# Performance work log

Measured on AMD Instinct MI355X. Metric: run time of the kernel, lower is better.

## Reference

```python
import jax, jax.numpy as jnp
import numpy as np

D_MODEL = 256   # per-head dim in this module
N_HEAD = 8
B, S = 4, 2048
NEG_INF = -1e9  # large negative in place of -inf for numerical safety


def setup_inputs() -> dict:
    key = jax.random.key(0)
    ks = jax.random.split(key, 8)
    d, h = D_MODEL, N_HEAD
    sc = 1.0 / np.sqrt(d)
    return {
        "Q": jax.random.normal(ks[0], (B, S, d), jnp.float32),
        "mask": jax.random.randint(ks[1], (B, S), 0, 2, jnp.int32),
        "WQ_w": jax.random.normal(ks[2], (h * d, d), jnp.float32) * sc,
        "WQ_b": jnp.zeros((h * d,), jnp.float32),
        "WK_w": jax.random.normal(ks[3], (h * d, d), jnp.float32) * sc,
        "WK_b": jnp.zeros((h * d,), jnp.float32),
        "WV_w": jax.random.normal(ks[4], (h * d, d), jnp.float32) * sc,
        "WV_b": jnp.zeros((h * d,), jnp.float32),
        "WO_w": jax.random.normal(ks[5], (d, h * d), jnp.float32) * sc,
        "WO_b": jnp.zeros((d,), jnp.float32),
        "ln_g": jnp.ones((d,), jnp.float32),
        "ln_b": jnp.zeros((d,), jnp.float32),
    }


def reference(Q, mask, WQ_w, WQ_b, WK_w, WK_b, WV_w, WV_b, WO_w, WO_b, ln_g, ln_b):
    b, s, d = Q.shape
    h = N_HEAD
    # projections (torch Linear: x @ W.T + b), split into heads: [b, h, s, d]
    q = (Q @ WQ_w.T + WQ_b).reshape(b, s, h, d).transpose(0, 2, 1, 3)
    k = (Q @ WK_w.T + WK_b).reshape(b, s, h, d).transpose(0, 2, 1, 3)
    v = (Q @ WV_w.T + WV_b).reshape(b, s, h, d).transpose(0, 2, 1, 3)
    # scaled dot-product scores [b, h, q, k]
    scores = jnp.einsum('bhqd,bhkd->bhqk', q, k) / jnp.sqrt(jnp.asarray(d, Q.dtype))
    key_mask = (mask != 0)[:, None, None, :]  # [b,1,1,k]
    scores = jnp.where(key_mask, scores, NEG_INF)
    alpha = jax.nn.softmax(scores, axis=-1)
    out = jnp.einsum('bhqk,bhkd->bhqd', alpha, v)
    out = out.transpose(0, 2, 1, 3).reshape(b, s, h * d)
    out = out @ WO_w.T + WO_b + Q  # dropout is identity in eval
    # LayerNorm over last dim
    mu = out.mean(-1, keepdims=True)
    var = out.var(-1, keepdims=True)
    return (out - mu) / jnp.sqrt(var + 1e-5) * ln_g + ln_b
```

## Files before the change

kernel.cpp:

```cpp
#include <hip/hip_runtime.h>
#include <cstddef>
#include <cstdint>

#define SQ 2048
#define DH 256
#define NH 8
#define BATCH 4
#define MROWS (BATCH*SQ)
#define HID (NH*DH)

typedef __attribute__((ext_vector_type(8)))  short bf16x8;
typedef __attribute__((ext_vector_type(16))) float f32x16;

typedef __attribute__((address_space(1))) const unsigned char gbuf_t;
typedef __attribute__((address_space(3))) unsigned char lbuf_t;

__device__ __forceinline__ void gl_lds16(const void* g, void* l) {
  __builtin_amdgcn_global_load_lds((gbuf_t*)g, (lbuf_t*)l, 16, 0, 0);
}

__device__ __forceinline__ unsigned short f2bf(float f) {
  unsigned u = __float_as_uint(f);
  unsigned r = (u + 0x7FFFu + ((u >> 16) & 1u)) >> 16;
  return (unsigned short)r;
}
__device__ __forceinline__ unsigned pk2(float a, float b) {
  return (unsigned)f2bf(a) | ((unsigned)f2bf(b) << 16);
}
__device__ __forceinline__ float fexp2(float x) {
  float r;
  asm("v_exp_f32 %0, %1" : "=v"(r) : "v"(x));
  return r;
}
__device__ __forceinline__ f32x16 zero16() {
  f32x16 v;
#pragma unroll
  for (int i = 0; i < 16; ++i) v[i] = 0.0f;
  return v;
}

__global__ void __launch_bounds__(256) cvt_kernel(
    const float* __restrict__ X,  const float* __restrict__ Wq,
    const float* __restrict__ Wk, const float* __restrict__ Wv,
    const float* __restrict__ Wo,
    unsigned short* __restrict__ Xb,  unsigned short* __restrict__ Wqb,
    unsigned short* __restrict__ Wkb, unsigned short* __restrict__ Wvb,
    unsigned short* __restrict__ Wob)
{
  int bid = blockIdx.x;
  const float* src; unsigned short* dst; size_t off;
  if      (bid < 512) { src = X;  dst = Xb;  off = (size_t)bid * 4096; }
  else if (bid < 640) { src = Wq; dst = Wqb; off = (size_t)(bid - 512) * 4096; }
  else if (bid < 768) { src = Wk; dst = Wkb; off = (size_t)(bid - 640) * 4096; }
  else if (bid < 896) { src = Wv; dst = Wvb; off = (size_t)(bid - 768) * 4096; }
  else                { src = Wo; dst = Wob; off = (size_t)(bid - 896) * 4096; }
  int tid = threadIdx.x;
#pragma unroll
  for (int k = 0; k < 4; ++k) {
    size_t idx = off + ((size_t)k * 256 + tid) * 4;
    float4 v = *(const float4*)(src + idx);
    uint2 o; o.x = pk2(v.x, v.y); o.y = pk2(v.z, v.w);
    *(uint2*)(dst + idx) = o;
  }
}

__global__ void __launch_bounds__(256, 2) qkv_kernel(
    const unsigned short* __restrict__ Xbf,
    const unsigned short* __restrict__ Wqb,
    const unsigned short* __restrict__ Wkb,
    const unsigned short* __restrict__ Wvb,
    const float* __restrict__ bq, const float* __restrict__ bk, const float* __restrict__ bv,
    unsigned short* __restrict__ q_ws, unsigned short* __restrict__ k_ws,
    unsigned short* __restrict__ vt_ws)
{
  __shared__ unsigned char TA[32768];
  __shared__ unsigned char TB[32768];
  const int tid = threadIdx.x, w = tid >> 6, l = tid & 63;
  const int h = l >> 5, t = l & 31;
  const int wm = w >> 1, wn = w & 1;
  const int z = blockIdx.z;
  const int m0 = (z == 2) ? blockIdx.y * 128 : blockIdx.x * 128;
  const int n0 = (z == 2) ? blockIdx.x * 128 : blockIdx.y * 128;
  const unsigned short* Asrc = (z == 2) ? Wvb : Xbf;
  const unsigned short* Bsrc = (z == 0) ? Wqb : (z == 1) ? Wkb : Xbf;

  const int rowo = l >> 4;
  const int bin  = (l & 15) * 16;
  const int swz  = (t & 15) << 4;

  f32x16 acc00 = zero16(), acc01 = zero16(), acc10 = zero16(), acc11 = zero16();

  for (int chunk = 0; chunk < 2; ++chunk) {
    __syncthreads();
#pragma unroll
    for (int i2 = 0; i2 < 8; ++i2) {
      int j = 8 * w + i2;
      int row = 4 * j + rowo;
      gl_lds16((const unsigned char*)(Asrc + (size_t)(m0 + row) * 256 + chunk * 128)
                 + (bin ^ ((row & 15) << 4)),
               &TA[j * 1024]);
    }
#pragma unroll
    for (int i2 = 0; i2 < 8; ++i2) {
      int j = 8 * w + i2;
      int row = 4 * j + rowo;
      gl_lds16((const unsigned char*)(Bsrc + (size_t)(n0 + row) * 256 + chunk * 128)
                 + (bin ^ ((row & 15) << 4)),
               &TB[j * 1024]);
    }
    __syncthreads();
#pragma unroll
    for (int kc = 0; kc < 8; ++kc) {
      int kb = (32 * kc + 16 * h) ^ swz;
      bf16x8 a0 = *(const bf16x8*)&TA[(size_t)(64 * wm + t) * 256 + kb];
      bf16x8 a1 = *(const bf16x8*)&TA[(size_t)(64 * wm + 32 + t) * 256 + kb];
      bf16x8 b0 = *(const bf16x8*)&TB[(size_t)(64 * wn + t) * 256 + kb];
      bf16x8 b1 = *(const bf16x8*)&TB[(size_t)(64 * wn + 32 + t) * 256 + kb];
      acc00 = __builtin_amdgcn_mfma_f32_32x32x16_bf16(a0, b0, acc00, 0, 0, 0);
      acc01 = __builtin_amdgcn_mfma_f32_32x32x16_bf16(a0, b1, acc01, 0, 0, 0);
      acc10 = __builtin_amdgcn_mfma_f32_32x32x16_bf16(a1, b0, acc10, 0, 0, 0);
      acc11 = __builtin_amdgcn_mfma_f32_32x32x16_bf16(a1, b1, acc11, 0, 0, 0);
    }
  }

  if (z < 2) {
    unsigned short* outp = z ? k_ws : q_ws;
    const float* bias = z ? bk : bq;
    float bn0 = bias[n0 + 64 * wn + t];
    float bn1 = bias[n0 + 64 * wn + 32 + t];
#pragma unroll
    for (int mt = 0; mt < 2; ++mt) {
#pragma unroll
      for (int nt = 0; nt < 2; ++nt) {
        int n = n0 + 64 * wn + 32 * nt + t;
        int headn = n >> 8, d = n & 255;
        float bb = nt ? bn1 : bn0;
        const f32x16& A = (mt == 0) ? (nt == 0 ? acc00 : acc01) : (nt == 0 ? acc10 : acc11);
#pragma unroll
        for (int r = 0; r < 16; ++r) {
          int m = m0 + 64 * wm + 32 * mt + (r & 3) + 8 * (r >> 2) + 4 * h;
          int batch = m >> 11, s = m & 2047;
          outp[(((size_t)batch * NH + headn) * SQ + s) * DH + d] = f2bf(A[r] + bb);
        }
      }
    }
  } else {
#pragma unroll
    for (int mt = 0; mt < 2; ++mt) {
#pragma unroll
      for (int r = 0; r < 16; ++r) {
        int j = m0 + 64 * wm + 32 * mt + (r & 3) + 8 * (r >> 2) + 4 * h;
        float bj = bv[j];
        int headj = j >> 8, jl = j & 255;
#pragma unroll
        for (int nt = 0; nt < 2; ++nt) {
          int sall = n0 + 64 * wn + 32 * nt + t;
          int batch = sall >> 11, ss = sall & 2047;
          const f32x16& A = (mt == 0) ? (nt == 0 ? acc00 : acc01) : (nt == 0 ? acc10 : acc11);
          vt_ws[((size_t)batch * NH + headj) * DH * SQ + (size_t)jl * SQ + ss] = f2bf(A[r] + bj);
        }
      }
    }
  }
}

__global__ void __launch_bounds__(512, 2) attn_kernel(
    const unsigned short* __restrict__ q_ws,
    const unsigned short* __restrict__ k_ws,
    const unsigned short* __restrict__ vt_ws,
    const int* __restrict__ mask,
    unsigned short* __restrict__ o_ws)
{
  __shared__ unsigned char KT[2][32768];
  __shared__ unsigned char VT[2][32768];
  __shared__ float MB[2048];

  const int tid = threadIdx.x, w = tid >> 6, l = tid & 63;
  const int h = l >> 5, t = l & 31;
  const int bid = blockIdx.x;
  const int xcd = bid & 7, slot = bid >> 3;
  const int bh = xcd * 4 + (slot >> 3);
  const int qt = slot & 7;
  const int b = bh >> 3, head = bh & 7;
  const int q0 = qt * 256;

  const float SC2 = 0.0625f * 1.44269504f;
  const float THR = 11.54f;

  {
    const int* mrow = mask + b * SQ;
    for (int i = tid; i < SQ; i += 512) MB[i] = mrow[i] ? 0.0f : -1.0e9f;
  }

  const unsigned short* kplane = k_ws + (size_t)bh * SQ * DH;
  const unsigned short* vplane = vt_ws + (size_t)bh * DH * SQ;

  bf16x8 qf[16];
  {
    const unsigned short* qb = q_ws + ((size_t)bh * SQ + (q0 + 32 * w + t)) * DH + 8 * h;
#pragma unroll
    for (int kc = 0; kc < 16; ++kc) qf[kc] = *(const bf16x8*)(qb + 16 * kc);
  }

  const int krow_o = l >> 5, kcol = (l & 31) * 16;
  const int vrow_o = l >> 3, vcol = (l & 7) * 16;

  {
#pragma unroll
    for (int i = 0; i < 4; ++i) {
      int j = 4 * w + i;
      int row = 2 * j + krow_o;
      gl_lds16((const unsigned char*)(kplane + (size_t)row * DH) + (kcol ^ ((row & 15) << 4)),
               &KT[0][j * 1024]);
    }
#pragma unroll
    for (int i = 0; i < 4; ++i) {
      int j = 4 * w + i;
      int row = 8 * j + vrow_o;
      gl_lds16((const unsigned char*)(vplane + (size_t)row * SQ) + (vcol ^ ((row & 7) << 4)),
               &VT[0][j * 1024]);
    }
  }
  __syncthreads();

  f32x16 o[8];
#pragma unroll
  for (int i = 0; i < 8; ++i) o[i] = zero16();
  float m_run = -3.0e38f, l_run = 0.0f;

  const int swzK = (t & 15) << 4;
  const int swzV = (t & 7) << 4;

  int cur = 0;
  for (int kb = 0; kb < SQ; kb += 64) {
    const int nxt = cur ^ 1;
    if (kb + 64 < SQ) {
#pragma unroll
      for (int i = 0; i < 4; ++i) {
        int j = 4 * w + i;
        int row = 2 * j + krow_o;
        gl_lds16((const unsigned char*)(kplane + (size_t)(kb + 64 + row) * DH) + (kcol ^ ((row & 15) << 4)),
                 &KT[nxt][j * 1024]);
      }
#pragma unroll
      for (int i = 0; i < 4; ++i) {
        int j = 4 * w + i;
        int row = 8 * j + vrow_o;
        gl_lds16((const unsigned char*)(vplane + (size_t)row * SQ + kb + 64) + (vcol ^ ((row & 7) << 4)),
                 &VT[nxt][j * 1024]);
      }
    }

    f32x16 sa0 = zero16(), sa1 = zero16();
    __builtin_amdgcn_s_setprio(1);
#pragma unroll
    for (int kc = 0; kc < 16; ++kc) {
      int kbb = (32 * kc + 16 * h) ^ swzK;
      bf16x8 a0 = *(const bf16x8*)&KT[cur][(size_t)t * 512 + kbb];
      bf16x8 a1 = *(const bf16x8*)&KT[cur][(size_t)(32 + t) * 512 + kbb];
      sa0 = __builtin_amdgcn_mfma_f32_32x32x16_bf16(a0, qf[kc], sa0, 0, 0, 0);
      sa1 = __builtin_amdgcn_mfma_f32_32x32x16_bf16(a1, qf[kc], sa1, 0, 0, 0);
    }
    __builtin_amdgcn_s_setprio(0);

#pragma unroll
    for (int g = 0; g < 4; ++g) {
      float4 m0v = *(const float4*)&MB[kb + 4 * h + 8 * g];
      float4 m1v = *(const float4*)&MB[kb + 32 + 4 * h + 8 * g];
      sa0[4*g+0] = sa0[4*g+0] * SC2 + m0v.x;
      sa0[4*g+1] = sa0[4*g+1] * SC2 + m0v.y;
      sa0[4*g+2] = sa0[4*g+2] * SC2 + m0v.z;
      sa0[4*g+3] = sa0[4*g+3] * SC2 + m0v.w;
      sa1[4*g+0] = sa1[4*g+0] * SC2 + m1v.x;
      sa1[4*g+1] = sa1[4*g+1] * SC2 + m1v.y;
      sa1[4*g+2] = sa1[4*g+2] * SC2 + m1v.z;
      sa1[4*g+3] = sa1[4*g+3] * SC2 + m1v.w;
    }
    f32x16 mm;
#pragma unroll
    for (int r = 0; r < 16; ++r) mm[r] = fmaxf(sa0[r], sa1[r]);
#pragma unroll
    for (int s = 8; s >= 1; s >>= 1) {
#pragma unroll
      for (int r = 0; r < 8; ++r) {
        if (r < s) mm[r] = fmaxf(mm[r], mm[r + s]);
      }
    }
    float tm = fmaxf(mm[0], __shfl_xor(mm[0], 32, 64));

    if (__builtin_expect(!__all(tm <= m_run + THR), 0)) {
      float m_new = fmaxf(m_run, tm);
      float rf = fexp2(m_run - m_new);
      m_run = m_new;
      l_run *= rf;
#pragma unroll
      for (int r = 0; r < 16; ++r) {
        float rr = __shfl(rf, (r & 3) + 8 * (r >> 2) + 4 * h, 64);
#pragma unroll
        for (int db = 0; db < 8; ++db) o[db][r] *= rr;
      }
    }

    float ssum = 0.0f;
#pragma unroll
    for (int ks = 0; ks < 4; ++ks) {
      const f32x16& P = (ks < 2) ? sa0 : sa1;
      const int base = 8 * (ks & 1);
      float e0 = fexp2(P[base + 0] - m_run);
      float e1 = fexp2(P[base + 1] - m_run);
      float e2 = fexp2(P[base + 2] - m_run);
      float e3 = fexp2(P[base + 3] - m_run);
      float e4 = fexp2(P[base + 4] - m_run);
      float e5 = fexp2(P[base + 5] - m_run);
      float e6 = fexp2(P[base + 6] - m_run);
      float e7 = fexp2(P[base + 7] - m_run);
      unsigned lo0, lo1, hi0, hi1;
      asm("v_cvt_pk_bf16_f32 %0, %1, %2" : "=v"(lo0) : "v"(e0), "v"(e1));
      asm("v_cvt_pk_bf16_f32 %0, %1, %2" : "=v"(lo1) : "v"(e2), "v"(e3));
      asm("v_cvt_pk_bf16_f32 %0, %1, %2" : "=v"(hi0) : "v"(e4), "v"(e5));
      asm("v_cvt_pk_bf16_f32 %0, %1, %2" : "=v"(hi1) : "v"(e6), "v"(e7));
      unsigned s0 = h ? lo0 : hi0;
      unsigned s1 = h ? lo1 : hi1;
      unsigned x0 = (unsigned)__shfl_xor((int)s0, 32, 64);
      unsigned x1 = (unsigned)__shfl_xor((int)s1, 32, 64);
      union { unsigned u[4]; bf16x8 v; } pu;
      pu.u[0] = h ? x0 : lo0;
      pu.u[1] = h ? x1 : lo1;
      pu.u[2] = h ? hi0 : x0;
      pu.u[3] = h ? hi1 : x1;
      bf16x8 pav = pu.v;
      ssum += ((e0 + e1) + (e2 + e3)) + ((e4 + e5) + (e6 + e7));
      __builtin_amdgcn_s_setprio(1);
#pragma unroll
      for (int db = 0; db < 8; ++db) {
        bf16x8 bv = *(const bf16x8*)&VT[cur][(size_t)(32 * db + t) * 128 + ((32 * ks + 16 * h) ^ swzV)];
        o[db] = __builtin_amdgcn_mfma_f32_32x32x16_bf16(pav, bv, o[db], 0, 0, 0);
      }
      __builtin_amdgcn_s_setprio(0);
    }
    float ls = ssum + __shfl_xor(ssum, 32, 64);
    l_run += ls;

    __syncthreads();
    cur = nxt;
  }

  float linv = 1.0f / l_run;
  unsigned short* ob = o_ws + (size_t)b * SQ * HID + (size_t)head * DH;
#pragma unroll
  for (int r = 0; r < 16; ++r) {
    int rowr = (r & 3) + 8 * (r >> 2) + 4 * h;
    float li = __shfl(linv, rowr, 64);
    int s = q0 + 32 * w + rowr;
    unsigned short* orow = ob + (size_t)s * HID;
#pragma unroll
    for (int db = 0; db < 8; ++db)
      orow[32 * db + t] = f2bf(o[db][r] * li);
  }
}

__global__ void __launch_bounds__(256, 2) oproj_ln_kernel(
    const unsigned short* __restrict__ Abf,
    const unsigned short* __restrict__ Wob,
    const float* __restrict__ bo, const float* __restrict__ Xin,
    const float* __restrict__ g, const float* __restrict__ be,
    float* __restrict__ out)
{
  __shared__ unsigned char TA[2][4096];
  __shared__ unsigned char TB[2][32768];
  __shared__ float RS1[4][32], RS2[4][32];
  const int tid = threadIdx.x, w = tid >> 6, l = tid & 63;
  const int h = l >> 5, t = l & 31;
  const int m0 = blockIdx.x * 32;
  const int arow_o = l >> 3, ab_in = (l & 7) * 16;
  const int swz = (t & 7) << 4;

  {
    int row = 8 * w + arow_o;
    gl_lds16((const unsigned char*)(Abf + (size_t)(m0 + row) * HID) + (ab_in ^ ((row & 7) << 4)),
             &TA[0][w * 1024]);
#pragma unroll
    for (int i2 = 0; i2 < 8; ++i2) {
      int j = 8 * w + i2;
      int row2 = 8 * j + arow_o;
      gl_lds16((const unsigned char*)(Wob + (size_t)row2 * HID) + (ab_in ^ ((row2 & 7) << 4)),
               &TB[0][j * 1024]);
    }
  }
  __syncthreads();

  f32x16 acc0 = zero16(), acc1 = zero16();
  int cur = 0;
  for (int chunk = 0; chunk < 32; ++chunk) {
    const int nxt = cur ^ 1;
    if (chunk + 1 < 32) {
      int row = 8 * w + arow_o;
      gl_lds16((const unsigned char*)(Abf + (size_t)(m0 + row) * HID + (chunk + 1) * 64) + (ab_in ^ ((row & 7) << 4)),
               &TA[nxt][w * 1024]);
#pragma unroll
      for (int i2 = 0; i2 < 8; ++i2) {
        int j = 8 * w + i2;
        int row2 = 8 * j + arow_o;
        gl_lds16((const unsigned char*)(Wob + (size_t)row2 * HID + (chunk + 1) * 64) + (ab_in ^ ((row2 & 7) << 4)),
                 &TB[nxt][j * 1024]);
      }
    }
#pragma unroll
    for (int kc = 0; kc < 4; ++kc) {
      int kbb = (32 * kc + 16 * h) ^ swz;
      bf16x8 a  = *(const bf16x8*)&TA[cur][(size_t)t * 128 + kbb];
      bf16x8 b0 = *(const bf16x8*)&TB[cur][(size_t)(64 * w + t) * 128 + kbb];
      bf16x8 b1 = *(const bf16x8*)&TB[cur][(size_t)(64 * w + 32 + t) * 128 + kbb];
      acc0 = __builtin_amdgcn_mfma_f32_32x32x16_bf16(a, b0, acc0, 0, 0, 0);
      acc1 = __builtin_amdgcn_mfma_f32_32x32x16_bf16(a, b1, acc1, 0, 0, 0);
    }
    __syncthreads();
    cur = nxt;
  }

  const int c0 = 64 * w + t, c1 = 64 * w + 32 + t;
  float bb0 = bo[c0], bb1 = bo[c1];
  float gc0 = g[c0],  gc1 = g[c1];
  float bc0 = be[c0], bc1 = be[c1];
#pragma unroll
  for (int r = 0; r < 16; ++r) {
    int row = m0 + (r & 3) + 8 * (r >> 2) + 4 * h;
    acc0[r] += bb0 + Xin[(size_t)row * DH + c0];
    acc1[r] += bb1 + Xin[(size_t)row * DH + c1];
  }

#pragma unroll
  for (int r = 0; r < 16; ++r) {
    float p1 = acc0[r] + acc1[r];
    float p2 = acc0[r] * acc0[r] + acc1[r] * acc1[r];
#pragma unroll
    for (int off = 1; off < 32; off <<= 1) {
      p1 += __shfl_xor(p1, off, 64);
      p2 += __shfl_xor(p2, off, 64);
    }
    if (t == 0) {
      int rl = (r & 3) + 8 * (r >> 2) + 4 * h;
      RS1[w][rl] = p1; RS2[w][rl] = p2;
    }
  }
  __syncthreads();

#pragma unroll
  for (int r = 0; r < 16; ++r) {
    int rl = (r & 3) + 8 * (r >> 2) + 4 * h;
    float s1 = (RS1[0][rl] + RS1[1][rl]) + (RS1[2][rl] + RS1[3][rl]);
    float s2 = (RS2[0][rl] + RS2[1][rl]) + (RS2[2][rl] + RS2[3][rl]);
    float mean = s1 * (1.0f / 256.0f);
    float var  = s2 * (1.0f / 256.0f) - mean * mean;
    float rstd = rsqrtf(var + 1e-5f);
    size_t rowo = (size_t)(m0 + rl) * DH;
    out[rowo + c0] = (acc0[r] - mean) * rstd * gc0 + bc0;
    out[rowo + c1] = (acc1[r] - mean) * rstd * gc1 + bc1;
  }
}

extern "C" void kernel_launch(void* const* d_in, const int* in_sizes, int n_in,
                              void* d_out, int out_size, void* d_ws, size_t ws_size,
                              hipStream_t stream) {
  const float* Q    = (const float*)d_in[0];
  const int*   mask = (const int*)  d_in[1];
  const float* WQ_w = (const float*)d_in[2];
  const float* WQ_b = (const float*)d_in[3];
  const float* WK_w = (const float*)d_in[4];
  const float* WK_b = (const float*)d_in[5];
  const float* WV_w = (const float*)d_in[6];
  const float* WV_b = (const float*)d_in[7];
  const float* WO_w = (const float*)d_in[8];
  const float* WO_b = (const float*)d_in[9];
  const float* ln_g = (const float*)d_in[10];
  const float* ln_b = (const float*)d_in[11];
  float* out = (float*)d_out;

  uint8_t* ws = (uint8_t*)d_ws;
  const size_t MB1 = 1048576;
  unsigned short* Xb   = (unsigned short*)(ws + 0 * MB1);
  unsigned short* Wqb  = (unsigned short*)(ws + 4 * MB1);
  unsigned short* Wkb  = (unsigned short*)(ws + 5 * MB1);
  unsigned short* Wvb  = (unsigned short*)(ws + 6 * MB1);
  unsigned short* Wob  = (unsigned short*)(ws + 7 * MB1);
  unsigned short* q_ws = (unsigned short*)(ws + 8 * MB1);
  unsigned short* k_ws = (unsigned short*)(ws + 40 * MB1);
  unsigned short* vtws = (unsigned short*)(ws + 72 * MB1);
  unsigned short* o_ws = (unsigned short*)(ws + 104 * MB1);

  cvt_kernel<<<1024, 256, 0, stream>>>(Q, WQ_w, WK_w, WV_w, WO_w, Xb, Wqb, Wkb, Wvb, Wob);
  qkv_kernel<<<dim3(64, 16, 3), 256, 0, stream>>>(Xb, Wqb, Wkb, Wvb, WQ_b, WK_b, WV_b,
                                                  q_ws, k_ws, vtws);
  attn_kernel<<<dim3(256), 512, 0, stream>>>(q_ws, k_ws, vtws, mask, o_ws);
  oproj_ln_kernel<<<dim3(256), 256, 0, stream>>>(o_ws, Wob, WO_b, Q, ln_g, ln_b, out);
}
```

Measured before the change: 283.8 us.

## Shrink attention tiles to 128 queries and 32-key blocks with 4-wave blocks

The attention kernel now runs 512 blocks of 256 threads, each handling 128 query rows, and streams K/V in 32-key blocks instead of 64. LDS buffers halve, and the QK^T product splits the head-dim reduction across two accumulators that are summed afterwards. The intent is better occupancy and load balance with less LDS per block. In exchange, each K/V tile is reused by fewer query rows, so there is more global traffic, and there are twice as many barriers and online-softmax rescale checks per key.

```diff
diff --git a/kernel.cpp b/kernel.cpp
--- a/kernel.cpp
+++ b/kernel.cpp
@@ -164,32 +164,32 @@
   }
 }
 
-__global__ void __launch_bounds__(512, 2) attn_kernel(
+__global__ void __launch_bounds__(256, 2) attn_kernel(
     const unsigned short* __restrict__ q_ws,
     const unsigned short* __restrict__ k_ws,
     const unsigned short* __restrict__ vt_ws,
     const int* __restrict__ mask,
     unsigned short* __restrict__ o_ws)
 {
-  __shared__ unsigned char KT[2][32768];
-  __shared__ unsigned char VT[2][32768];
+  __shared__ unsigned char KT[2][16384];
+  __shared__ unsigned char VT[2][16384];
   __shared__ float MB[2048];
 
   const int tid = threadIdx.x, w = tid >> 6, l = tid & 63;
   const int h = l >> 5, t = l & 31;
   const int bid = blockIdx.x;
   const int xcd = bid & 7, slot = bid >> 3;
-  const int bh = xcd * 4 + (slot >> 3);
-  const int qt = slot & 7;
+  const int bh = xcd * 4 + (slot >> 4);
+  const int qt = slot & 15;
   const int b = bh >> 3, head = bh & 7;
-  const int q0 = qt * 256;
+  const int q0 = qt * 128;
 
   const float SC2 = 0.0625f * 1.44269504f;
   const float THR = 11.54f;
 
   {
     const int* mrow = mask + b * SQ;
-    for (int i = tid; i < SQ; i += 512) MB[i] = mrow[i] ? 0.0f : -1.0e9f;
+    for (int i = tid; i < SQ; i += 256) MB[i] = mrow[i] ? 0.0f : -1.0e9f;
   }
 
   const unsigned short* kplane = k_ws + (size_t)bh * SQ * DH;
@@ -203,7 +203,7 @@
   }
 
   const int krow_o = l >> 5, kcol = (l & 31) * 16;
-  const int vrow_o = l >> 3, vcol = (l & 7) * 16;
+  const int vrow_o = l >> 2, vcol = (l & 3) * 16;
 
   {
 #pragma unroll
@@ -216,8 +216,8 @@
 #pragma unroll
     for (int i = 0; i < 4; ++i) {
       int j = 4 * w + i;
-      int row = 8 * j + vrow_o;
-      gl_lds16((const unsigned char*)(vplane + (size_t)row * SQ) + (vcol ^ ((row & 7) << 4)),
+      int row = 16 * j + vrow_o;
+      gl_lds16((const unsigned char*)(vplane + (size_t)row * SQ) + (vcol ^ ((row & 3) << 4)),
                &VT[0][j * 1024]);
     }
   }
@@ -229,56 +229,50 @@
   float m_run = -3.0e38f, l_run = 0.0f;
 
   const int swzK = (t & 15) << 4;
-  const int swzV = (t & 7) << 4;
+  const int swzV = (t & 3) << 4;
 
   int cur = 0;
-  for (int kb = 0; kb < SQ; kb += 64) {
+  for (int kb = 0; kb < SQ; kb += 32) {
     const int nxt = cur ^ 1;
-    if (kb + 64 < SQ) {
+    if (kb + 32 < SQ) {
 #pragma unroll
       for (int i = 0; i < 4; ++i) {
         int j = 4 * w + i;
         int row = 2 * j + krow_o;
-        gl_lds16((const unsigned char*)(kplane + (size_t)(kb + 64 + row) * DH) + (kcol ^ ((row & 15) << 4)),
+        gl_lds16((const unsigned char*)(kplane + (size_t)(kb + 32 + row) * DH) + (kcol ^ ((row & 15) << 4)),
                  &KT[nxt][j * 1024]);
       }
 #pragma unroll
       for (int i = 0; i < 4; ++i) {
         int j = 4 * w + i;
-        int row = 8 * j + vrow_o;
-        gl_lds16((const unsigned char*)(vplane + (size_t)row * SQ + kb + 64) + (vcol ^ ((row & 7) << 4)),
+        int row = 16 * j + vrow_o;
+        gl_lds16((const unsigned char*)(vplane + (size_t)row * SQ + kb + 32) + (vcol ^ ((row & 3) << 4)),
                  &VT[nxt][j * 1024]);
       }
     }
 
-    f32x16 sa0 = zero16(), sa1 = zero16();
+    f32x16 sa = zero16(), sb = zero16();
     __builtin_amdgcn_s_setprio(1);
 #pragma unroll
-    for (int kc = 0; kc < 16; ++kc) {
-      int kbb = (32 * kc + 16 * h) ^ swzK;
-      bf16x8 a0 = *(const bf16x8*)&KT[cur][(size_t)t * 512 + kbb];
-      bf16x8 a1 = *(const bf16x8*)&KT[cur][(size_t)(32 + t) * 512 + kbb];
-      sa0 = __builtin_amdgcn_mfma_f32_32x32x16_bf16(a0, qf[kc], sa0, 0, 0, 0);
-      sa1 = __builtin_amdgcn_mfma_f32_32x32x16_bf16(a1, qf[kc], sa1, 0, 0, 0);
+    for (int kc = 0; kc < 8; ++kc) {
+      int kbbA = (32 * (2 * kc) + 16 * h) ^ swzK;
+      int kbbB = (32 * (2 * kc + 1) + 16 * h) ^ swzK;
+      bf16x8 a0 = *(const bf16x8*)&KT[cur][(size_t)t * 512 + kbbA];
+      bf16x8 a1 = *(const bf16x8*)&KT[cur][(size_t)t * 512 + kbbB];
+      sa = __builtin_amdgcn_mfma_f32_32x32x16_bf16(a0, qf[2 * kc], sa, 0, 0, 0);
+      sb = __builtin_amdgcn_mfma_f32_32x32x16_bf16(a1, qf[2 * kc + 1], sb, 0, 0, 0);
     }
     __builtin_amdgcn_s_setprio(0);
 
 #pragma unroll
     for (int g = 0; g < 4; ++g) {
       float4 m0v = *(const float4*)&MB[kb + 4 * h + 8 * g];
-      float4 m1v = *(const float4*)&MB[kb + 32 + 4 * h + 8 * g];
-      sa0[4*g+0] = sa0[4*g+0] * SC2 + m0v.x;
-      sa0[4*g+1] = sa0[4*g+1] * SC2 + m0v.y;
-      sa0[4*g+2] = sa0[4*g+2] * SC2 + m0v.z;
-      sa0[4*g+3] = sa0[4*g+3] * SC2 + m0v.w;
-      sa1[4*g+0] = sa1[4*g+0] * SC2 + m1v.x;
-      sa1[4*g+1] = sa1[4*g+1] * SC2 + m1v.y;
-      sa1[4*g+2] = sa1[4*g+2] * SC2 + m1v.z;
-      sa1[4*g+3] = sa1[4*g+3] * SC2 + m1v.w;
-    }
-    f32x16 mm;
-#pragma unroll
-    for (int r = 0; r < 16; ++r) mm[r] = fmaxf(sa0[r], sa1[r]);
+      sa[4*g+0] = (sa[4*g+0] + sb[4*g+0]) * SC2 + m0v.x;
+      sa[4*g+1] = (sa[4*g+1] + sb[4*g+1]) * SC2 + m0v.y;
+      sa[4*g+2] = (sa[4*g+2] + sb[4*g+2]) * SC2 + m0v.z;
+      sa[4*g+3] = (sa[4*g+3] + sb[4*g+3]) * SC2 + m0v.w;
+    }
+    f32x16 mm = sa;
 #pragma unroll
     for (int s = 8; s >= 1; s >>= 1) {
 #pragma unroll
@@ -303,17 +297,16 @@
 
     float ssum = 0.0f;
 #pragma unroll
-    for (int ks = 0; ks < 4; ++ks) {
-      const f32x16& P = (ks < 2) ? sa0 : sa1;
-      const int base = 8 * (ks & 1);
-      float e0 = fexp2(P[base + 0] - m_run);
-      float e1 = fexp2(P[base + 1] - m_run);
-      float e2 = fexp2(P[base + 2] - m_run);
-      float e3 = fexp2(P[base + 3] - m_run);
-      float e4 = fexp2(P[base + 4] - m_run);
-      float e5 = fexp2(P[base + 5] - m_run);
-      float e6 = fexp2(P[base + 6] - m_run);
-      float e7 = fexp2(P[base + 7] - m_run);
+    for (int ks = 0; ks < 2; ++ks) {
+      const int base = 8 * ks;
+      float e0 = fexp2(sa[base + 0] - m_run);
+      float e1 = fexp2(sa[base + 1] - m_run);
+      float e2 = fexp2(sa[base + 2] - m_run);
+      float e3 = fexp2(sa[base + 3] - m_run);
+      float e4 = fexp2(sa[base + 4] - m_run);
+      float e5 = fexp2(sa[base + 5] - m_run);
+      float e6 = fexp2(sa[base + 6] - m_run);
+      float e7 = fexp2(sa[base + 7] - m_run);
       unsigned lo0, lo1, hi0, hi1;
       asm("v_cvt_pk_bf16_f32 %0, %1, %2" : "=v"(lo0) : "v"(e0), "v"(e1));
       asm("v_cvt_pk_bf16_f32 %0, %1, %2" : "=v"(lo1) : "v"(e2), "v"(e3));
@@ -333,7 +326,7 @@
       __builtin_amdgcn_s_setprio(1);
 #pragma unroll
       for (int db = 0; db < 8; ++db) {
-        bf16x8 bv = *(const bf16x8*)&VT[cur][(size_t)(32 * db + t) * 128 + ((32 * ks + 16 * h) ^ swzV)];
+        bf16x8 bv = *(const bf16x8*)&VT[cur][(size_t)(32 * db + t) * 64 + ((32 * ks + 16 * h) ^ swzV)];
         o[db] = __builtin_amdgcn_mfma_f32_32x32x16_bf16(pav, bv, o[db], 0, 0, 0);
       }
       __builtin_amdgcn_s_setprio(0);
@@ -491,6 +484,6 @@
   cvt_kernel<<<1024, 256, 0, stream>>>(Q, WQ_w, WK_w, WV_w, WO_w, Xb, Wqb, Wkb, Wvb, Wob);
   qkv_kernel<<<dim3(64, 16, 3), 256, 0, stream>>>(Xb, Wqb, Wkb, Wvb, WQ_b, WK_b, WV_b,
                                                   q_ws, k_ws, vtws);
-  attn_kernel<<<dim3(256), 512, 0, stream>>>(q_ws, k_ws, vtws, mask, o_ws);
+  attn_kernel<<<dim3(512), 256, 0, stream>>>(q_ws, k_ws, vtws, mask, o_ws);
   oproj_ln_kernel<<<dim3(256), 256, 0, stream>>>(o_ws, Wob, WO_b, Q, ln_g, ln_b, out);
 }
```

After: 319.8 us. +12.7%, slower.
